# Performance work log

Hardware: AMD Instinct MI355X
Metric: run time of the kernel (lower is better)

Reference implementation:

```python
import jax, jax.numpy as jnp
import numpy as np

EPS = 1e-06


def reference(x, gamma):
    # x: [B, C, W, H] feature map; gamma: [1] learned scale
    B, C, W, H = x.shape
    N = W * H
    V = x.reshape(B, C, N)                       # Q = K = V = flattened x
    # l2 norm over channel dim (dim=-2) per spatial position -> [B, N]
    inv_norm = 1.0 / jnp.linalg.norm(V, axis=-2)  # [B, N]
    Qn = V * inv_norm[:, None, :]                 # [B, C, N]
    Kt = jnp.swapaxes(Qn, -1, -2)                 # [B, N, C] (K normalized, transposed)
    # Taylor-softmax denominator: 1 / (N + K^T . (sum_c Q + eps))
    q_colsum = jnp.sum(Qn, axis=-2) + EPS         # [B, N]
    tailor_sum = 1.0 / (N + jnp.einsum('bnc,bn->bc', Kt, q_colsum))  # [B, C]
    # sum of V over channels, broadcast over channels -> [B, C, N]
    value_sum = jnp.sum(V, axis=-2)[:, None, :]   # [B, 1, N]
    # linear-attention reordering: (V K^T) Q, cost O(B C^2 N)
    matrix = jnp.einsum('bcn,bnm->bcm', V, Kt)            # [B, C, C]
    matrix_sum = value_sum + jnp.einsum('bcm,bmn->bcn', matrix, Qn)  # [B, C, N]
    weight_value = matrix_sum * tailor_sum[:, :, None]    # [B, C, N]
    weight_value = weight_value.reshape(B, C, W, H)
    return x + gamma * weight_value


def setup_inputs() -> dict:
    key = jax.random.key(0)
    k1, k2 = jax.random.split(key)
    x = jax.random.normal(k1, (8, 512, 128, 128), dtype=jnp.float32)
    gamma = jax.random.uniform(k2, (1,), dtype=jnp.float32)
    return {"x": x, "gamma": gamma}
```

## Files before the change

kernel.cpp:

```cpp
#include <hip/hip_runtime.h>
#include <hip/hip_bf16.h>

#define B_ 8
#define C_ 512
#define N_ 16384
#define EPSF 1e-6f
#define KSPLIT1 16
#define NTILES1 10

typedef float f32x4 __attribute__((ext_vector_type(4)));
typedef short s16x8 __attribute__((ext_vector_type(8)));
typedef short s16x4 __attribute__((ext_vector_type(4)));

__device__ __forceinline__ short f2bf(float f) {
  union { float f; unsigned u; } v; v.f = f;
  unsigned r = v.u + 0x7fffu + ((v.u >> 16) & 1u);
  return (short)(r >> 16);
}

__device__ __forceinline__ s16x8 pack8(f32x4 a, f32x4 b) {
  s16x8 r;
  r[0] = f2bf(a[0]); r[1] = f2bf(a[1]); r[2] = f2bf(a[2]); r[3] = f2bf(a[3]);
  r[4] = f2bf(b[0]); r[5] = f2bf(b[1]); r[6] = f2bf(b[2]); r[7] = f2bf(b[3]);
  return r;
}

__device__ __forceinline__ void mfma16(f32x4& d, s16x8 a, s16x8 b) {
  asm("v_mfma_f32_16x16x32_bf16 %0, %1, %2, %0" : "+v"(d) : "v"(a), "v"(b));
}

#define GLOAD16(gp, lp)                                                        \
  __builtin_amdgcn_global_load_lds(                                            \
      (const __attribute__((address_space(1))) unsigned int*)(gp),             \
      (__attribute__((address_space(3))) unsigned int*)(lp), 16, 0, 0)

__global__ __launch_bounds__(256) void k_stats(const float* __restrict__ x,
                                               float* __restrict__ inv,
                                               float* __restrict__ csum) {
  __shared__ f32x4 ssm[4][64];
  __shared__ f32x4 csm[4][64];
  int t = threadIdx.x, nq = t & 63, cs = t >> 6;
  int g0 = blockIdx.x * 256 + nq * 4;
  int b = g0 >> 14;
  int n = g0 & (N_ - 1);
  const float* p = x + ((size_t)b * C_ + cs * 128) * N_ + n;
  f32x4 ss = {0.f, 0.f, 0.f, 0.f}, sc = {0.f, 0.f, 0.f, 0.f};
  for (int c = 0; c < 128; ++c) {
    f32x4 v = *(const f32x4*)(p + (size_t)c * N_);
    ss += v * v;
    sc += v;
  }
  ssm[cs][nq] = ss; csm[cs][nq] = sc;
  __syncthreads();
  if (t < 64) {
    f32x4 s1 = ssm[0][t] + ssm[1][t] + ssm[2][t] + ssm[3][t];
    f32x4 c1 = csm[0][t] + csm[1][t] + csm[2][t] + csm[3][t];
    f32x4 r;
#pragma unroll
    for (int j = 0; j < 4; ++j) r[j] = 1.0f / sqrtf(s1[j]);
    int g = blockIdx.x * 256 + t * 4;
    *(f32x4*)(inv + g) = r;
    *(f32x4*)(csum + g) = c1;
  }
}

__global__ __launch_bounds__(256) void k_conv(const float* __restrict__ x,
                                              const float* __restrict__ inv,
                                              const float* __restrict__ csum,
                                              short* __restrict__ W,
                                              short* __restrict__ QnT,
                                              float* __restrict__ tpart) {
  __shared__ float tp[16][128];
  int bid = blockIdx.x;
  int nblk = bid & 127; bid >>= 7;
  int cblk = bid & 3; bid >>= 2;
  int b = bid;
  int t = threadIdx.x, cg = t & 15, ng = t >> 4;
  int c0 = cblk * 128 + cg * 8;
  int n0 = nblk * 128 + ng * 8;
  const float* xb = x + ((size_t)b * C_ + c0) * N_ + n0;
  const float* ivp = inv + (size_t)b * N_ + n0;
  const float* csp = csum + (size_t)b * N_ + n0;
  float iv[8], rs[8], t2[8];
  {
    f32x4 ia = *(const f32x4*)ivp, ib = *(const f32x4*)(ivp + 4);
    f32x4 ca = *(const f32x4*)csp, cb = *(const f32x4*)(csp + 4);
#pragma unroll
    for (int j = 0; j < 4; ++j) {
      iv[j] = ia[j]; iv[4 + j] = ib[j];
      t2[j] = fmaf(ca[j], ia[j], EPSF);
      t2[4 + j] = fmaf(cb[j], ib[j], EPSF);
    }
#pragma unroll
    for (int j = 0; j < 8; ++j) rs[j] = sqrtf(iv[j]);
  }
  short* Wb = W + ((size_t)b * C_ + c0) * N_ + n0;
  s16x8 qcol[8];
#pragma unroll
  for (int i = 0; i < 8; ++i) {
    f32x4 a = *(const f32x4*)(xb + (size_t)i * N_);
    f32x4 bb = *(const f32x4*)(xb + (size_t)i * N_ + 4);
    s16x8 wv;
    float s = 0.f;
#pragma unroll
    for (int j = 0; j < 4; ++j) {
      float v = a[j];
      wv[j] = f2bf(v * rs[j]);
      float q = v * iv[j];
      qcol[j][i] = f2bf(q);
      s = fmaf(q, t2[j], s);
    }
#pragma unroll
    for (int j = 0; j < 4; ++j) {
      float v = bb[j];
      wv[4 + j] = f2bf(v * rs[4 + j]);
      float q = v * iv[4 + j];
      qcol[4 + j][i] = f2bf(q);
      s = fmaf(q, t2[4 + j], s);
    }
    *(s16x8*)(Wb + (size_t)i * N_) = wv;
    tp[ng][cg * 8 + i] = s;
  }
  short* Qb = QnT + ((size_t)b * N_ + n0) * C_ + c0;
#pragma unroll
  for (int j = 0; j < 8; ++j) *(s16x8*)(Qb + (size_t)j * C_) = qcol[j];
  __syncthreads();
  if (t < 128) {
    float s = 0.f;
#pragma unroll
    for (int g = 0; g < 16; ++g) s += tp[g][t];
    tpart[((size_t)b * C_ + cblk * 128 + t) * 128 + nblk] = s;
  }
}

__global__ __launch_bounds__(256) void k_tailor2(const float* __restrict__ tpart,
                                                 float* __restrict__ tail) {
  int i = blockIdx.x * 256 + threadIdx.x;
  const float* p = tpart + (size_t)i * 128;
  f32x4 s4 = {0.f, 0.f, 0.f, 0.f};
#pragma unroll
  for (int k = 0; k < 32; ++k) s4 += *(const f32x4*)(p + k * 4);
  tail[i] = 1.0f / ((float)N_ + s4[0] + s4[1] + s4[2] + s4[3]);
}

__global__ __launch_bounds__(256) void k_gemm1(const short* __restrict__ W,
                                               float* __restrict__ matP) {
  __shared__ __align__(16) short As[8192];
  __shared__ __align__(16) short Bs[8192];
  const int TI[NTILES1] = {0, 0, 0, 0, 1, 1, 1, 2, 2, 3};
  const int TJ[NTILES1] = {0, 1, 2, 3, 1, 2, 3, 2, 3, 3};
  int bid = blockIdx.x;
  int ks = bid & 15; bid >>= 4;
  int tt = bid % NTILES1;
  int b = bid / NTILES1;
  int mt = TI[tt], nt = TJ[tt];

  int t = threadIdx.x, lane = t & 63, w = t >> 6;
  int wr = w >> 1, wc = w & 1;
  int prow0 = lane >> 3;
  int swz = ((lane & 7) * 16) ^ (prow0 << 4);

  const short* Wb = W + (size_t)b * C_ * N_;
  const char* gA[4]; const char* gB[4];
  short* lA[4]; short* lB[4];
#pragma unroll
  for (int cc = 0; cc < 4; ++cc) {
    int q = w * 4 + cc;
    int row = q * 8 + prow0;
    gA[cc] = (const char*)(Wb + (size_t)(mt * 128 + row) * N_) + swz;
    gB[cc] = (const char*)(Wb + (size_t)(nt * 128 + row) * N_) + swz;
    lA[cc] = &As[q * 512];
    lB[cc] = &Bs[q * 512];
  }

  f32x4 acc[4][4];
#pragma unroll
  for (int i = 0; i < 4; ++i)
#pragma unroll
    for (int j = 0; j < 4; ++j) acc[i][j] = f32x4{0.f, 0.f, 0.f, 0.f};

  int kbeg = ks * (N_ / KSPLIT1);
  for (int kk = 0; kk < N_ / KSPLIT1; kk += 64) {
    __syncthreads();
    size_t koff = (size_t)(kbeg + kk) * 2;
#pragma unroll
    for (int cc = 0; cc < 4; ++cc) GLOAD16(gA[cc] + koff, lA[cc]);
#pragma unroll
    for (int cc = 0; cc < 4; ++cc) GLOAD16(gB[cc] + koff, lB[cc]);
    __syncthreads();
#pragma unroll
    for (int h = 0; h < 2; ++h) {
      int kb = h * 64 + (lane >> 4) * 16;
      s16x8 af[4], bf[4];
#pragma unroll
      for (int mi = 0; mi < 4; ++mi) {
        int row = wr * 64 + mi * 16 + (lane & 15);
        af[mi] = *(const s16x8*)((const char*)As + row * 128 + (kb ^ ((row & 7) << 4)));
      }
#pragma unroll
      for (int ni = 0; ni < 4; ++ni) {
        int row = wc * 64 + ni * 16 + (lane & 15);
        bf[ni] = *(const s16x8*)((const char*)Bs + row * 128 + (kb ^ ((row & 7) << 4)));
      }
#pragma unroll
      for (int mi = 0; mi < 4; ++mi)
#pragma unroll
        for (int ni = 0; ni < 4; ++ni) mfma16(acc[mi][ni], af[mi], bf[ni]);
    }
  }
  asm volatile("s_nop 7\n\ts_nop 7\n\ts_nop 7" ::);
  float* mp = matP + (((size_t)ks * B_ + b) * NTILES1 + tt) * 16384;
#pragma unroll
  for (int mi = 0; mi < 4; ++mi)
#pragma unroll
    for (int ni = 0; ni < 4; ++ni) {
      int col = wc * 64 + ni * 16 + (lane & 15);
#pragma unroll
      for (int r = 0; r < 4; ++r) {
        int row = wr * 64 + mi * 16 + (lane >> 4) * 4 + r;
        mp[(size_t)row * 128 + col] = acc[mi][ni][r];
      }
    }
}

__global__ __launch_bounds__(256) void k_redsum2(const float* __restrict__ matP,
                                                 short* __restrict__ matF) {
  const int TI[NTILES1] = {0, 0, 0, 0, 1, 1, 1, 2, 2, 3};
  const int TJ[NTILES1] = {0, 1, 2, 3, 1, 2, 3, 2, 3, 3};
  size_t idx = (size_t)blockIdx.x * 256 + threadIdx.x;
  int b = (int)(idx / (NTILES1 * 16384));
  int rem = (int)(idx % (NTILES1 * 16384));
  int tt = rem >> 14;
  int e = rem & 16383;
  int rowl = e >> 7, col = e & 127;
  float s = 0.f;
#pragma unroll
  for (int ks = 0; ks < KSPLIT1; ++ks)
    s += matP[(((size_t)ks * B_ + b) * NTILES1 + tt) * 16384 + e];
  short v = f2bf(s);
  int ti = TI[tt], tj = TJ[tt];
  short* mb = matF + (size_t)b * C_ * C_;
  mb[(size_t)(ti * 128 + rowl) * C_ + tj * 128 + col] = v;
  if (ti != tj) mb[(size_t)(tj * 128 + col) * C_ + ti * 128 + rowl] = v;
}

__global__ __launch_bounds__(512) void k_gemm2(const float* __restrict__ x,
                                               const short* __restrict__ matF,
                                               const short* __restrict__ QnT,
                                               const float* __restrict__ csum,
                                               const float* __restrict__ tail,
                                               const float* __restrict__ gamma,
                                               float* __restrict__ out) {
  __shared__ __align__(16) short As[8192];
  __shared__ __align__(16) short Bs[16384];
  int bid = blockIdx.x;
  int nt = bid & 63; bid >>= 6;
  int mt = bid & 3; bid >>= 2;
  int b = bid;

  int t = threadIdx.x, lane = t & 63, w = t >> 6;
  int wrm = w >> 2, wcn = w & 3;
  int prow0 = lane >> 3;
  int swz = ((lane & 7) * 16) ^ (prow0 << 4);

  const char* gA[2]; short* lA[2];
  const char* gB[4]; short* lB[4];
#pragma unroll
  for (int i = 0; i < 2; ++i) {
    int row = i * 64 + w * 8 + prow0;
    gA[i] = (const char*)(matF + ((size_t)b * C_ + mt * 128 + row) * C_) + swz;
    lA[i] = &As[(i * 64 + w * 8) * 64];
  }
#pragma unroll
  for (int i = 0; i < 4; ++i) {
    int row = i * 64 + w * 8 + prow0;
    gB[i] = (const char*)(QnT + ((size_t)b * N_ + nt * 256 + row) * C_) + swz;
    lB[i] = &Bs[(i * 64 + w * 8) * 64];
  }

  f32x4 acc[4][4];
#pragma unroll
  for (int i = 0; i < 4; ++i)
#pragma unroll
    for (int j = 0; j < 4; ++j) acc[i][j] = f32x4{0.f, 0.f, 0.f, 0.f};

  for (int kk = 0; kk < C_; kk += 64) {
    __syncthreads();
    size_t koff = (size_t)kk * 2;
#pragma unroll
    for (int i = 0; i < 2; ++i) GLOAD16(gA[i] + koff, lA[i]);
#pragma unroll
    for (int i = 0; i < 4; ++i) GLOAD16(gB[i] + koff, lB[i]);
    __syncthreads();
#pragma unroll
    for (int h = 0; h < 2; ++h) {
      int kb = h * 64 + (lane >> 4) * 16;
      s16x8 af[4], bf[4];
#pragma unroll
      for (int mi = 0; mi < 4; ++mi) {
        int row = wrm * 64 + mi * 16 + (lane & 15);
        af[mi] = *(const s16x8*)((const char*)As + row * 128 + (kb ^ ((row & 7) << 4)));
      }
#pragma unroll
      for (int ni = 0; ni < 4; ++ni) {
        int row = wcn * 64 + ni * 16 + (lane & 15);
        bf[ni] = *(const s16x8*)((const char*)Bs + row * 128 + (kb ^ ((row & 7) << 4)));
      }
#pragma unroll
      for (int mi = 0; mi < 4; ++mi)
#pragma unroll
        for (int ni = 0; ni < 4; ++ni) mfma16(acc[mi][ni], af[mi], bf[ni]);
    }
  }
  asm volatile("s_nop 7\n\ts_nop 7\n\ts_nop 7" ::);
  float g = gamma[0];
#pragma unroll
  for (int mi = 0; mi < 4; ++mi)
#pragma unroll
    for (int ni = 0; ni < 4; ++ni) {
      int coln = nt * 256 + wcn * 64 + ni * 16 + (lane & 15);
      float vs = csum[(size_t)b * N_ + coln];
#pragma unroll
      for (int r = 0; r < 4; ++r) {
        int rowg = mt * 128 + wrm * 64 + mi * 16 + (lane >> 4) * 4 + r;
        float ts = tail[b * C_ + rowg];
        size_t off = ((size_t)b * C_ + rowg) * N_ + coln;
        out[off] = x[off] + g * ((vs + acc[mi][ni][r]) * ts);
      }
    }
}

__global__ __launch_bounds__(256) void k_tailor_fb(const float* __restrict__ x,
                                                   const float* __restrict__ inv,
                                                   const float* __restrict__ csum,
                                                   float* __restrict__ tail) {
  int b = blockIdx.x >> 9;
  const float* row = x + (size_t)blockIdx.x * N_;
  const float* ib = inv + b * N_;
  const float* cb = csum + b * N_;
  int t = threadIdx.x;
  float acc = 0.f;
  for (int i = t * 4; i < N_; i += 1024) {
    f32x4 v = *(const f32x4*)(row + i);
    f32x4 iv = *(const f32x4*)(ib + i);
    f32x4 cv = *(const f32x4*)(cb + i);
#pragma unroll
    for (int j = 0; j < 4; ++j) acc += v[j] * (iv[j] * fmaf(iv[j], cv[j], EPSF));
  }
#pragma unroll
  for (int off = 32; off > 0; off >>= 1) acc += __shfl_down(acc, off, 64);
  __shared__ float red[4];
  if ((t & 63) == 0) red[t >> 6] = acc;
  __syncthreads();
  if (t == 0) tail[blockIdx.x] = 1.0f / ((float)N_ + red[0] + red[1] + red[2] + red[3]);
}

__global__ __launch_bounds__(256) void k_gemm1_fb(const float* __restrict__ x,
                                                  const float* __restrict__ inv,
                                                  float* __restrict__ mpart,
                                                  int ksplit) {
  __shared__ short As[128 * 40];
  __shared__ short Bs[128 * 40];
  int bid = blockIdx.x;
  int ks = bid % ksplit; bid /= ksplit;
  int nt = bid & 3; bid >>= 2;
  int mt = bid & 3; bid >>= 2;
  int b = bid;
  int kch = N_ / ksplit;
  int kbeg = ks * kch, kend = kbeg + kch;
  int t = threadIdx.x, lane = t & 63, w = t >> 6, wr = w >> 1, wc = w & 1;
  int srow = t >> 1, skh = t & 1;
  const float* xb = x + (size_t)b * C_ * N_;
  const float* ga = xb + (size_t)(mt * 128 + srow) * N_ + skh * 16;
  const float* gb = xb + (size_t)(nt * 128 + srow) * N_ + skh * 16;
  const float* gi = inv + b * N_ + skh * 16;
  f32x4 acc[4][4];
#pragma unroll
  for (int i = 0; i < 4; ++i)
#pragma unroll
    for (int j = 0; j < 4; ++j) acc[i][j] = f32x4{0.f, 0.f, 0.f, 0.f};
  int ldsw = srow * 40 + skh * 16;
  int lra = (wr * 64 + (lane & 15)) * 40 + (lane >> 4) * 8;
  int lrb = (wc * 64 + (lane & 15)) * 40 + (lane >> 4) * 8;
  for (int kk = kbeg; kk < kend; kk += 32) {
    __syncthreads();
    {
      f32x4 a0 = *(const f32x4*)(ga + kk), a1 = *(const f32x4*)(ga + kk + 4);
      f32x4 a2 = *(const f32x4*)(ga + kk + 8), a3 = *(const f32x4*)(ga + kk + 12);
      f32x4 b0 = *(const f32x4*)(gb + kk), b1 = *(const f32x4*)(gb + kk + 4);
      f32x4 b2 = *(const f32x4*)(gb + kk + 8), b3 = *(const f32x4*)(gb + kk + 12);
      f32x4 i0 = *(const f32x4*)(gi + kk), i1 = *(const f32x4*)(gi + kk + 4);
      f32x4 i2 = *(const f32x4*)(gi + kk + 8), i3 = *(const f32x4*)(gi + kk + 12);
      *(s16x8*)&As[ldsw] = pack8(a0, a1);
      *(s16x8*)&As[ldsw + 8] = pack8(a2, a3);
      *(s16x8*)&Bs[ldsw] = pack8(b0 * i0, b1 * i1);
      *(s16x8*)&Bs[ldsw + 8] = pack8(b2 * i2, b3 * i3);
    }
    __syncthreads();
    s16x8 af[4], bf[4];
#pragma unroll
    for (int mi = 0; mi < 4; ++mi) af[mi] = *(const s16x8*)&As[lra + mi * 16 * 40];
#pragma unroll
    for (int ni = 0; ni < 4; ++ni) bf[ni] = *(const s16x8*)&Bs[lrb + ni * 16 * 40];
#pragma unroll
    for (int mi = 0; mi < 4; ++mi)
#pragma unroll
      for (int ni = 0; ni < 4; ++ni) mfma16(acc[mi][ni], af[mi], bf[ni]);
  }
  asm volatile("s_nop 7\n\ts_nop 7\n\ts_nop 7" ::);
  float* mp = mpart + ((size_t)ks * B_ + b) * C_ * C_;
#pragma unroll
  for (int mi = 0; mi < 4; ++mi)
#pragma unroll
    for (int ni = 0; ni < 4; ++ni) {
      int col = nt * 128 + wc * 64 + ni * 16 + (lane & 15);
#pragma unroll
      for (int r = 0; r < 4; ++r) {
        int rowg = mt * 128 + wr * 64 + mi * 16 + (lane >> 4) * 4 + r;
        mp[(size_t)rowg * C_ + col] = acc[mi][ni][r];
      }
    }
}

__global__ __launch_bounds__(256) void k_reduce_fb(const float* __restrict__ mpart,
                                                   float* __restrict__ mfull,
                                                   int ksplit) {
  size_t i = (size_t)blockIdx.x * 256 + threadIdx.x;
  float s = 0.f;
  for (int k = 0; k < ksplit; ++k) s += mpart[(size_t)k * (B_ * C_ * C_) + i];
  mfull[i] = s;
}

__global__ __launch_bounds__(256) void k_gemm2_fb(const float* __restrict__ x,
                                                  const float* __restrict__ mat,
                                                  const float* __restrict__ inv,
                                                  const float* __restrict__ csum,
                                                  const float* __restrict__ tail,
                                                  const float* __restrict__ gamma,
                                                  float* __restrict__ out) {
  __shared__ short As[128 * 40];
  __shared__ short Bs[128 * 40];
  int bid = blockIdx.x;
  int nt = bid & 127; bid >>= 7;
  int mt = bid & 3; bid >>= 2;
  int b = bid;
  int t = threadIdx.x, lane = t & 63, w = t >> 6, wr = w >> 1, wc = w & 1;
  int srow = t >> 1, skh = t & 1;
  const float* gA = mat + ((size_t)b * C_ + mt * 128 + srow) * C_ + skh * 16;
  int kb = t >> 5, cbl = t & 31;
  int k0l = kb * 4, n0 = cbl * 4;
  const float* xb = x + (size_t)b * C_ * N_;
  const float* gB = xb + (size_t)k0l * N_ + nt * 128 + n0;
  f32x4 ivn = *(const f32x4*)(inv + b * N_ + nt * 128 + n0);
  f32x4 acc[4][4];
#pragma unroll
  for (int i = 0; i < 4; ++i)
#pragma unroll
    for (int j = 0; j < 4; ++j) acc[i][j] = f32x4{0.f, 0.f, 0.f, 0.f};
  int ldsw = srow * 40 + skh * 16;
  int lra = (wr * 64 + (lane & 15)) * 40 + (lane >> 4) * 8;
  int lrb = (wc * 64 + (lane & 15)) * 40 + (lane >> 4) * 8;
  for (int kk = 0; kk < C_; kk += 32) {
    __syncthreads();
    {
      f32x4 a0 = *(const f32x4*)(gA + kk), a1 = *(const f32x4*)(gA + kk + 4);
      f32x4 a2 = *(const f32x4*)(gA + kk + 8), a3 = *(const f32x4*)(gA + kk + 12);
      *(s16x8*)&As[ldsw] = pack8(a0, a1);
      *(s16x8*)&As[ldsw + 8] = pack8(a2, a3);
      const float* pB = gB + (size_t)kk * N_;
      f32x4 v0 = *(const f32x4*)(pB);
      f32x4 v1 = *(const f32x4*)(pB + N_);
      f32x4 v2 = *(const f32x4*)(pB + 2 * N_);
      f32x4 v3 = *(const f32x4*)(pB + 3 * N_);
#pragma unroll
      for (int cc = 0; cc < 4; ++cc) {
        s16x4 q;
        q[0] = f2bf(v0[cc] * ivn[cc]);
        q[1] = f2bf(v1[cc] * ivn[cc]);
        q[2] = f2bf(v2[cc] * ivn[cc]);
        q[3] = f2bf(v3[cc] * ivn[cc]);
        *(s16x4*)&Bs[(n0 + cc) * 40 + k0l] = q;
      }
    }
    __syncthreads();
    s16x8 af[4], bf[4];
#pragma unroll
    for (int mi = 0; mi < 4; ++mi) af[mi] = *(const s16x8*)&As[lra + mi * 16 * 40];
#pragma unroll
    for (int ni = 0; ni < 4; ++ni) bf[ni] = *(const s16x8*)&Bs[lrb + ni * 16 * 40];
#pragma unroll
    for (int mi = 0; mi < 4; ++mi)
#pragma unroll
      for (int ni = 0; ni < 4; ++ni) mfma16(acc[mi][ni], af[mi], bf[ni]);
  }
  asm volatile("s_nop 7\n\ts_nop 7\n\ts_nop 7" ::);
  float g = gamma[0];
#pragma unroll
  for (int mi = 0; mi < 4; ++mi)
#pragma unroll
    for (int ni = 0; ni < 4; ++ni) {
      int coln = nt * 128 + wc * 64 + ni * 16 + (lane & 15);
      float vs = csum[b * N_ + coln];
#pragma unroll
      for (int r = 0; r < 4; ++r) {
        int rowg = mt * 128 + wr * 64 + mi * 16 + (lane >> 4) * 4 + r;
        float ts = tail[b * C_ + rowg];
        size_t off = ((size_t)b * C_ + rowg) * N_ + coln;
        out[off] = x[off] + g * ((vs + acc[mi][ni][r]) * ts);
      }
    }
}

extern "C" void kernel_launch(void* const* d_in, const int* in_sizes, int n_in,
                              void* d_out, int out_size, void* d_ws, size_t ws_size,
                              hipStream_t stream) {
  const float* x = (const float*)d_in[0];
  const float* gamma = (const float*)d_in[1];
  float* out = (float*)d_out;
  float* wsf = (float*)d_ws;

  const size_t needA = 141574144ull;
  if (ws_size >= needA) {
    float* inv = wsf;
    float* csum = wsf + 131072;
    float* tail = wsf + 262144;
    float* tpart = wsf + 266240;
    short* matF = (short*)(wsf + 790528);
    short* QnT = (short*)(wsf + 1839104);
    short* W = (short*)d_out;
    float* matP = (float*)d_out + 33554432ull;

    k_stats<<<512, 256, 0, stream>>>(x, inv, csum);
    k_conv<<<4096, 256, 0, stream>>>(x, inv, csum, W, QnT, tpart);
    k_tailor2<<<16, 256, 0, stream>>>(tpart, tail);
    k_gemm1<<<B_ * NTILES1 * KSPLIT1, 256, 0, stream>>>(W, matP);
    k_redsum2<<<(B_ * NTILES1 * 16384) / 256, 256, 0, stream>>>(matP, matF);
    k_gemm2<<<2048, 512, 0, stream>>>(x, matF, QnT, csum, tail, gamma, out);
  } else {
    float* inv = wsf;
    float* csum = wsf + 131072;
    float* tail = wsf + 262144;
    float* matP = wsf + 266240;
    int ksplit = (ws_size >= 43008000ull) ? 4 : 1;
    float* matF = (ksplit > 1) ? (matP + (size_t)ksplit * 2097152) : matP;

    k_stats<<<512, 256, 0, stream>>>(x, inv, csum);
    k_tailor_fb<<<B_ * C_, 256, 0, stream>>>(x, inv, csum, tail);
    k_gemm1_fb<<<B_ * 16 * ksplit, 256, 0, stream>>>(x, inv, matP, ksplit);
    if (ksplit > 1) k_reduce_fb<<<8192, 256, 0, stream>>>(matP, matF, ksplit);
    k_gemm2_fb<<<B_ * 4 * 128, 256, 0, stream>>>(x, matF, inv, csum, tail, gamma, out);
  }
}
```

Before: 410.1 us.

## Double-buffer LDS tiles in both GEMMs and retile gemm2 to 128x128

```diff
diff --git a/kernel.cpp b/kernel.cpp
--- a/kernel.cpp
+++ b/kernel.cpp
@@ -145,8 +145,8 @@
 
 __global__ __launch_bounds__(256) void k_gemm1(const short* __restrict__ W,
                                                float* __restrict__ matP) {
-  __shared__ __align__(16) short As[8192];
-  __shared__ __align__(16) short Bs[8192];
+  __shared__ __align__(16) short As[2][8192];
+  __shared__ __align__(16) short Bs[2][8192];
   const int TI[NTILES1] = {0, 0, 0, 0, 1, 1, 1, 2, 2, 3};
   const int TJ[NTILES1] = {0, 1, 2, 3, 1, 2, 3, 2, 3, 3};
   int bid = blockIdx.x;
@@ -161,16 +161,16 @@
   int swz = ((lane & 7) * 16) ^ (prow0 << 4);
 
   const short* Wb = W + (size_t)b * C_ * N_;
+  size_t kbyte = (size_t)(ks * (N_ / KSPLIT1)) * 2;
   const char* gA[4]; const char* gB[4];
-  short* lA[4]; short* lB[4];
+  int lofs[4];
 #pragma unroll
   for (int cc = 0; cc < 4; ++cc) {
     int q = w * 4 + cc;
     int row = q * 8 + prow0;
-    gA[cc] = (const char*)(Wb + (size_t)(mt * 128 + row) * N_) + swz;
-    gB[cc] = (const char*)(Wb + (size_t)(nt * 128 + row) * N_) + swz;
-    lA[cc] = &As[q * 512];
-    lB[cc] = &Bs[q * 512];
+    gA[cc] = (const char*)(Wb + (size_t)(mt * 128 + row) * N_) + swz + kbyte;
+    gB[cc] = (const char*)(Wb + (size_t)(nt * 128 + row) * N_) + swz + kbyte;
+    lofs[cc] = q * 512;
   }
 
   f32x4 acc[4][4];
@@ -179,15 +179,26 @@
 #pragma unroll
     for (int j = 0; j < 4; ++j) acc[i][j] = f32x4{0.f, 0.f, 0.f, 0.f};
 
-  int kbeg = ks * (N_ / KSPLIT1);
-  for (int kk = 0; kk < N_ / KSPLIT1; kk += 64) {
-    __syncthreads();
-    size_t koff = (size_t)(kbeg + kk) * 2;
-#pragma unroll
-    for (int cc = 0; cc < 4; ++cc) GLOAD16(gA[cc] + koff, lA[cc]);
-#pragma unroll
-    for (int cc = 0; cc < 4; ++cc) GLOAD16(gB[cc] + koff, lB[cc]);
-    __syncthreads();
+#define STG1(pb, kof)                                                          \
+  do {                                                                         \
+    _Pragma("unroll")                                                          \
+    for (int cc = 0; cc < 4; ++cc) GLOAD16(gA[cc] + (kof), &As[pb][lofs[cc]]); \
+    _Pragma("unroll")                                                          \
+    for (int cc = 0; cc < 4; ++cc) GLOAD16(gB[cc] + (kof), &Bs[pb][lofs[cc]]); \
+  } while (0)
+
+  STG1(0, 0);
+#pragma unroll
+  for (int tk = 0; tk < 16; ++tk) {
+    if (tk < 15) {
+      STG1((tk + 1) & 1, (size_t)(tk + 1) * 128);
+      asm volatile("s_waitcnt vmcnt(8)" ::: "memory");
+    } else {
+      asm volatile("s_waitcnt vmcnt(0)" ::: "memory");
+    }
+    asm volatile("s_barrier" ::: "memory");
+    const char* pA = (const char*)As[tk & 1];
+    const char* pB = (const char*)Bs[tk & 1];
 #pragma unroll
     for (int h = 0; h < 2; ++h) {
       int kb = h * 64 + (lane >> 4) * 16;
@@ -195,19 +206,21 @@
 #pragma unroll
       for (int mi = 0; mi < 4; ++mi) {
         int row = wr * 64 + mi * 16 + (lane & 15);
-        af[mi] = *(const s16x8*)((const char*)As + row * 128 + (kb ^ ((row & 7) << 4)));
+        af[mi] = *(const s16x8*)(pA + row * 128 + (kb ^ ((row & 7) << 4)));
       }
 #pragma unroll
       for (int ni = 0; ni < 4; ++ni) {
         int row = wc * 64 + ni * 16 + (lane & 15);
-        bf[ni] = *(const s16x8*)((const char*)Bs + row * 128 + (kb ^ ((row & 7) << 4)));
+        bf[ni] = *(const s16x8*)(pB + row * 128 + (kb ^ ((row & 7) << 4)));
       }
 #pragma unroll
       for (int mi = 0; mi < 4; ++mi)
 #pragma unroll
         for (int ni = 0; ni < 4; ++ni) mfma16(acc[mi][ni], af[mi], bf[ni]);
     }
-  }
+    asm volatile("s_barrier" ::: "memory");
+  }
+#undef STG1
   asm volatile("s_nop 7\n\ts_nop 7\n\ts_nop 7" ::);
   float* mp = matP + (((size_t)ks * B_ + b) * NTILES1 + tt) * 16384;
 #pragma unroll
@@ -244,38 +257,34 @@
   if (ti != tj) mb[(size_t)(tj * 128 + col) * C_ + ti * 128 + rowl] = v;
 }
 
-__global__ __launch_bounds__(512) void k_gemm2(const float* __restrict__ x,
+__global__ __launch_bounds__(256) void k_gemm2(const float* __restrict__ x,
                                                const short* __restrict__ matF,
                                                const short* __restrict__ QnT,
                                                const float* __restrict__ csum,
                                                const float* __restrict__ tail,
                                                const float* __restrict__ gamma,
                                                float* __restrict__ out) {
-  __shared__ __align__(16) short As[8192];
-  __shared__ __align__(16) short Bs[16384];
+  __shared__ __align__(16) short As[2][8192];
+  __shared__ __align__(16) short Bs[2][8192];
   int bid = blockIdx.x;
-  int nt = bid & 63; bid >>= 6;
+  int nt = bid & 127; bid >>= 7;
   int mt = bid & 3; bid >>= 2;
   int b = bid;
 
   int t = threadIdx.x, lane = t & 63, w = t >> 6;
-  int wrm = w >> 2, wcn = w & 3;
+  int wr = w >> 1, wc = w & 1;
   int prow0 = lane >> 3;
   int swz = ((lane & 7) * 16) ^ (prow0 << 4);
 
-  const char* gA[2]; short* lA[2];
-  const char* gB[4]; short* lB[4];
-#pragma unroll
-  for (int i = 0; i < 2; ++i) {
-    int row = i * 64 + w * 8 + prow0;
-    gA[i] = (const char*)(matF + ((size_t)b * C_ + mt * 128 + row) * C_) + swz;
-    lA[i] = &As[(i * 64 + w * 8) * 64];
-  }
-#pragma unroll
-  for (int i = 0; i < 4; ++i) {
-    int row = i * 64 + w * 8 + prow0;
-    gB[i] = (const char*)(QnT + ((size_t)b * N_ + nt * 256 + row) * C_) + swz;
-    lB[i] = &Bs[(i * 64 + w * 8) * 64];
+  const char* gA[4]; const char* gB[4];
+  int lofs[4];
+#pragma unroll
+  for (int cc = 0; cc < 4; ++cc) {
+    int q = w * 4 + cc;
+    int row = q * 8 + prow0;
+    gA[cc] = (const char*)(matF + ((size_t)b * C_ + mt * 128 + row) * C_) + swz;
+    gB[cc] = (const char*)(QnT + ((size_t)b * N_ + nt * 128 + row) * C_) + swz;
+    lofs[cc] = q * 512;
   }
 
   f32x4 acc[4][4];
@@ -284,45 +293,59 @@
 #pragma unroll
     for (int j = 0; j < 4; ++j) acc[i][j] = f32x4{0.f, 0.f, 0.f, 0.f};
 
-  for (int kk = 0; kk < C_; kk += 64) {
-    __syncthreads();
-    size_t koff = (size_t)kk * 2;
-#pragma unroll
-    for (int i = 0; i < 2; ++i) GLOAD16(gA[i] + koff, lA[i]);
-#pragma unroll
-    for (int i = 0; i < 4; ++i) GLOAD16(gB[i] + koff, lB[i]);
-    __syncthreads();
+#define STG2(pb, kof)                                                          \
+  do {                                                                         \
+    _Pragma("unroll")                                                          \
+    for (int cc = 0; cc < 4; ++cc) GLOAD16(gA[cc] + (kof), &As[pb][lofs[cc]]); \
+    _Pragma("unroll")                                                          \
+    for (int cc = 0; cc < 4; ++cc) GLOAD16(gB[cc] + (kof), &Bs[pb][lofs[cc]]); \
+  } while (0)
+
+  STG2(0, 0);
+#pragma unroll
+  for (int tk = 0; tk < 8; ++tk) {
+    if (tk < 7) {
+      STG2((tk + 1) & 1, (size_t)(tk + 1) * 128);
+      asm volatile("s_waitcnt vmcnt(8)" ::: "memory");
+    } else {
+      asm volatile("s_waitcnt vmcnt(0)" ::: "memory");
+    }
+    asm volatile("s_barrier" ::: "memory");
+    const char* pA = (const char*)As[tk & 1];
+    const char* pB = (const char*)Bs[tk & 1];
 #pragma unroll
     for (int h = 0; h < 2; ++h) {
       int kb = h * 64 + (lane >> 4) * 16;
       s16x8 af[4], bf[4];
 #pragma unroll
       for (int mi = 0; mi < 4; ++mi) {
-        int row = wrm * 64 + mi * 16 + (lane & 15);
-        af[mi] = *(const s16x8*)((const char*)As + row * 128 + (kb ^ ((row & 7) << 4)));
+        int row = wr * 64 + mi * 16 + (lane & 15);
+        af[mi] = *(const s16x8*)(pA + row * 128 + (kb ^ ((row & 7) << 4)));
       }
 #pragma unroll
       for (int ni = 0; ni < 4; ++ni) {
-        int row = wcn * 64 + ni * 16 + (lane & 15);
-        bf[ni] = *(const s16x8*)((const char*)Bs + row * 128 + (kb ^ ((row & 7) << 4)));
+        int row = wc * 64 + ni * 16 + (lane & 15);
+        bf[ni] = *(const s16x8*)(pB + row * 128 + (kb ^ ((row & 7) << 4)));
       }
 #pragma unroll
       for (int mi = 0; mi < 4; ++mi)
 #pragma unroll
         for (int ni = 0; ni < 4; ++ni) mfma16(acc[mi][ni], af[mi], bf[ni]);
     }
-  }
+    asm volatile("s_barrier" ::: "memory");
+  }
+#undef STG2
   asm volatile("s_nop 7\n\ts_nop 7\n\ts_nop 7" ::);
   float g = gamma[0];
 #pragma unroll
   for (int mi = 0; mi < 4; ++mi)
 #pragma unroll
     for (int ni = 0; ni < 4; ++ni) {
-      int coln = nt * 256 + wcn * 64 + ni * 16 + (lane & 15);
+      int coln = nt * 128 + wc * 64 + ni * 16 + (lane & 15);
       float vs = csum[(size_t)b * N_ + coln];
 #pragma unroll
       for (int r = 0; r < 4; ++r) {
-        int rowg = mt * 128 + wrm * 64 + mi * 16 + (lane >> 4) * 4 + r;
+        int rowg = mt * 128 + wr * 64 + mi * 16 + (lane >> 4) * 4 + r;
         float ts = tail[b * C_ + rowg];
         size_t off = ((size_t)b * C_ + rowg) * N_ + coln;
         out[off] = x[off] + g * ((vs + acc[mi][ni][r]) * ts);
@@ -535,7 +558,7 @@
     k_tailor2<<<16, 256, 0, stream>>>(tpart, tail);
     k_gemm1<<<B_ * NTILES1 * KSPLIT1, 256, 0, stream>>>(W, matP);
     k_redsum2<<<(B_ * NTILES1 * 16384) / 256, 256, 0, stream>>>(matP, matF);
-    k_gemm2<<<2048, 512, 0, stream>>>(x, matF, QnT, csum, tail, gamma, out);
+    k_gemm2<<<4096, 256, 0, stream>>>(x, matF, QnT, csum, tail, gamma, out);
   } else {
     float* inv = wsf;
     float* csum = wsf + 131072;
```

Result: slower. 433.1 us (+5.6%).

## Double-buffer LDS in second GEMM and halve N tile for higher occupancy

Applied to the files above, without the earlier changes.

```diff
diff --git a/kernel.cpp b/kernel.cpp
--- a/kernel.cpp
+++ b/kernel.cpp
@@ -244,85 +244,95 @@
   if (ti != tj) mb[(size_t)(tj * 128 + col) * C_ + ti * 128 + rowl] = v;
 }
 
-__global__ __launch_bounds__(512) void k_gemm2(const float* __restrict__ x,
-                                               const short* __restrict__ matF,
-                                               const short* __restrict__ QnT,
-                                               const float* __restrict__ csum,
-                                               const float* __restrict__ tail,
-                                               const float* __restrict__ gamma,
-                                               float* __restrict__ out) {
-  __shared__ __align__(16) short As[8192];
-  __shared__ __align__(16) short Bs[16384];
+__global__ __launch_bounds__(512, 4) void k_gemm2(const float* __restrict__ x,
+                                                  const short* __restrict__ matF,
+                                                  const short* __restrict__ QnT,
+                                                  const float* __restrict__ csum,
+                                                  const float* __restrict__ tail,
+                                                  const float* __restrict__ gamma,
+                                                  float* __restrict__ out) {
+  __shared__ __align__(16) short As[2][8192];
+  __shared__ __align__(16) short Bs[2][8192];
   int bid = blockIdx.x;
-  int nt = bid & 63; bid >>= 6;
+  int nt = bid & 127; bid >>= 7;
   int mt = bid & 3; bid >>= 2;
   int b = bid;
 
   int t = threadIdx.x, lane = t & 63, w = t >> 6;
-  int wrm = w >> 2, wcn = w & 3;
+  int wr = w >> 2, wc = w & 3;
   int prow0 = lane >> 3;
   int swz = ((lane & 7) * 16) ^ (prow0 << 4);
 
-  const char* gA[2]; short* lA[2];
-  const char* gB[4]; short* lB[4];
-#pragma unroll
-  for (int i = 0; i < 2; ++i) {
-    int row = i * 64 + w * 8 + prow0;
-    gA[i] = (const char*)(matF + ((size_t)b * C_ + mt * 128 + row) * C_) + swz;
-    lA[i] = &As[(i * 64 + w * 8) * 64];
-  }
-#pragma unroll
-  for (int i = 0; i < 4; ++i) {
-    int row = i * 64 + w * 8 + prow0;
-    gB[i] = (const char*)(QnT + ((size_t)b * N_ + nt * 256 + row) * C_) + swz;
-    lB[i] = &Bs[(i * 64 + w * 8) * 64];
-  }
-
-  f32x4 acc[4][4];
+  const char* gA[2]; const char* gB[2];
+  int lofs[2];
+#pragma unroll
+  for (int cc = 0; cc < 2; ++cc) {
+    int q = w * 2 + cc;
+    int row = q * 8 + prow0;
+    gA[cc] = (const char*)(matF + ((size_t)b * C_ + mt * 128 + row) * C_) + swz;
+    gB[cc] = (const char*)(QnT + ((size_t)b * N_ + nt * 128 + row) * C_) + swz;
+    lofs[cc] = q * 512;
+  }
+
+  f32x4 acc[4][2];
 #pragma unroll
   for (int i = 0; i < 4; ++i)
 #pragma unroll
-    for (int j = 0; j < 4; ++j) acc[i][j] = f32x4{0.f, 0.f, 0.f, 0.f};
-
-  for (int kk = 0; kk < C_; kk += 64) {
-    __syncthreads();
-    size_t koff = (size_t)kk * 2;
-#pragma unroll
-    for (int i = 0; i < 2; ++i) GLOAD16(gA[i] + koff, lA[i]);
-#pragma unroll
-    for (int i = 0; i < 4; ++i) GLOAD16(gB[i] + koff, lB[i]);
-    __syncthreads();
+    for (int j = 0; j < 2; ++j) acc[i][j] = f32x4{0.f, 0.f, 0.f, 0.f};
+
+#define STG2(pb, kof)                                                          \
+  do {                                                                         \
+    _Pragma("unroll")                                                          \
+    for (int cc = 0; cc < 2; ++cc) GLOAD16(gA[cc] + (kof), &As[pb][lofs[cc]]); \
+    _Pragma("unroll")                                                          \
+    for (int cc = 0; cc < 2; ++cc) GLOAD16(gB[cc] + (kof), &Bs[pb][lofs[cc]]); \
+  } while (0)
+
+  STG2(0, 0);
+#pragma unroll
+  for (int tk = 0; tk < 8; ++tk) {
+    if (tk < 7) {
+      STG2((tk + 1) & 1, (size_t)(tk + 1) * 128);
+      asm volatile("s_waitcnt vmcnt(4)" ::: "memory");
+    } else {
+      asm volatile("s_waitcnt vmcnt(0)" ::: "memory");
+    }
+    asm volatile("s_barrier" ::: "memory");
+    const char* pA = (const char*)As[tk & 1];
+    const char* pB = (const char*)Bs[tk & 1];
 #pragma unroll
     for (int h = 0; h < 2; ++h) {
       int kb = h * 64 + (lane >> 4) * 16;
-      s16x8 af[4], bf[4];
+      s16x8 af[4], bf[2];
 #pragma unroll
       for (int mi = 0; mi < 4; ++mi) {
-        int row = wrm * 64 + mi * 16 + (lane & 15);
-        af[mi] = *(const s16x8*)((const char*)As + row * 128 + (kb ^ ((row & 7) << 4)));
-      }
-#pragma unroll
-      for (int ni = 0; ni < 4; ++ni) {
-        int row = wcn * 64 + ni * 16 + (lane & 15);
-        bf[ni] = *(const s16x8*)((const char*)Bs + row * 128 + (kb ^ ((row & 7) << 4)));
+        int row = wr * 64 + mi * 16 + (lane & 15);
+        af[mi] = *(const s16x8*)(pA + row * 128 + (kb ^ ((row & 7) << 4)));
+      }
+#pragma unroll
+      for (int ni = 0; ni < 2; ++ni) {
+        int row = wc * 32 + ni * 16 + (lane & 15);
+        bf[ni] = *(const s16x8*)(pB + row * 128 + (kb ^ ((row & 7) << 4)));
       }
 #pragma unroll
       for (int mi = 0; mi < 4; ++mi)
 #pragma unroll
-        for (int ni = 0; ni < 4; ++ni) mfma16(acc[mi][ni], af[mi], bf[ni]);
-    }
-  }
+        for (int ni = 0; ni < 2; ++ni) mfma16(acc[mi][ni], af[mi], bf[ni]);
+    }
+    asm volatile("s_barrier" ::: "memory");
+  }
+#undef STG2
   asm volatile("s_nop 7\n\ts_nop 7\n\ts_nop 7" ::);
   float g = gamma[0];
 #pragma unroll
   for (int mi = 0; mi < 4; ++mi)
 #pragma unroll
-    for (int ni = 0; ni < 4; ++ni) {
-      int coln = nt * 256 + wcn * 64 + ni * 16 + (lane & 15);
+    for (int ni = 0; ni < 2; ++ni) {
+      int coln = nt * 128 + wc * 32 + ni * 16 + (lane & 15);
       float vs = csum[(size_t)b * N_ + coln];
 #pragma unroll
       for (int r = 0; r < 4; ++r) {
-        int rowg = mt * 128 + wrm * 64 + mi * 16 + (lane >> 4) * 4 + r;
+        int rowg = mt * 128 + wr * 64 + mi * 16 + (lane >> 4) * 4 + r;
         float ts = tail[b * C_ + rowg];
         size_t off = ((size_t)b * C_ + rowg) * N_ + coln;
         out[off] = x[off] + g * ((vs + acc[mi][ni][r]) * ts);
@@ -535,7 +545,7 @@
     k_tailor2<<<16, 256, 0, stream>>>(tpart, tail);
     k_gemm1<<<B_ * NTILES1 * KSPLIT1, 256, 0, stream>>>(W, matP);
     k_redsum2<<<(B_ * NTILES1 * 16384) / 256, 256, 0, stream>>>(matP, matF);
-    k_gemm2<<<2048, 512, 0, stream>>>(x, matF, QnT, csum, tail, gamma, out);
+    k_gemm2<<<4096, 512, 0, stream>>>(x, matF, QnT, csum, tail, gamma, out);
   } else {
     float* inv = wsf;
     float* csum = wsf + 131072;
```

Result: no change. 416.7 us (+1.6%).
